# Optimization experiments

Hardware: AMD Instinct MI355X
Metric: run time of the kernel (lower is better)

## Reference

```python
import jax, jax.numpy as jnp
import numpy as np

B, N, C = 2, 2048, 1024
H = 16
HD = C // H
GH = C // 4  # spatial gate hidden dim


def setup_inputs() -> dict:
    key = jax.random.key(0)
    ks = jax.random.split(key, 10)
    s = 0.02
    return {
        "x": jax.random.normal(ks[0], (B, N, C), dtype=jnp.float32),
        "spatial_mask": jax.random.uniform(ks[1], (B, N), dtype=jnp.float32),
        # qkv Linear: weight [3C, C], bias [3C] (torch convention: y = x @ W.T + b)
        "qkv_w": jax.random.normal(ks[2], (3 * C, C), dtype=jnp.float32) * s,
        "qkv_b": jnp.zeros((3 * C,), dtype=jnp.float32),
        # output proj Linear: weight [C, C], bias [C]
        "proj_w": jax.random.normal(ks[3], (C, C), dtype=jnp.float32) * s,
        "proj_b": jnp.zeros((C,), dtype=jnp.float32),
        # spatial_gate: Linear(1, C//4) -> ReLU -> Linear(C//4, 1) -> Sigmoid
        "g1_w": jax.random.normal(ks[4], (GH, 1), dtype=jnp.float32) * 0.5,
        "g1_b": jnp.zeros((GH,), dtype=jnp.float32),
        "g2_w": jax.random.normal(ks[5], (1, GH), dtype=jnp.float32) * 0.1,
        "g2_b": jnp.zeros((1,), dtype=jnp.float32),
    }


def reference(x, spatial_mask, qkv_w, qkv_b, proj_w, proj_b, g1_w, g1_b, g2_w, g2_b):
    b, n, c = x.shape
    # QKV projection: [B, N, 3C] -> [3, B, H, N, HD]
    qkv = (x @ qkv_w.T + qkv_b).reshape(b, n, 3, H, HD).transpose(2, 0, 3, 1, 4)
    q, k, v = qkv[0], qkv[1], qkv[2]

    # scaled attention scores [B, H, N, N]
    attn = jnp.einsum("bhqd,bhkd->bhqk", q, k) * (HD ** -0.5)

    # spatial gate on the mask: scalar MLP applied per key position
    m = spatial_mask[..., None]                      # [B, N, 1]
    h = jax.nn.relu(m @ g1_w.T + g1_b)               # [B, N, GH]
    gate = jax.nn.sigmoid(h @ g2_w.T + g2_b)         # [B, N, 1]
    gate = gate[:, None, None, :, 0]                 # [B, 1, 1, N] broadcasts over heads & queries

    attn = jax.nn.softmax(attn * gate, axis=-1)

    out = jnp.einsum("bhqk,bhkd->bhqd", attn, v)     # [B, H, N, HD]
    out = out.transpose(0, 2, 1, 3).reshape(b, n, c) # [B, N, C]
    return out @ proj_w.T + proj_b
```

## Files before the change

### kernel.cpp

```cpp
#include <hip/hip_runtime.h>

#define H 16
#define NSEQ 2048
#define HD 64
#define CDIM 1024

typedef __attribute__((ext_vector_type(8))) short s8v;
typedef __attribute__((ext_vector_type(4))) float f4v;
typedef __attribute__((ext_vector_type(16))) float f16v;

#define GLL(g, l) __builtin_amdgcn_global_load_lds( \
    (const __attribute__((address_space(1))) void*)(g), \
    (__attribute__((address_space(3))) void*)(l), 16, 0, 0)

__device__ __forceinline__ short f2bf(float f) {
  union { float f; unsigned u; } x; x.f = f;
  unsigned r = (x.u + 0x7fffu + ((x.u >> 16) & 1u)) >> 16;
  return (short)r;
}
__device__ __forceinline__ short f2bf_fast(float f) {
  return (short)((__float_as_uint(f) + 0x8000u) >> 16);
}
__device__ __forceinline__ unsigned pk(float a, float b) {
  unsigned ua = __float_as_uint(a) + 0x8000u;
  unsigned ub = __float_as_uint(b) + 0x8000u;
  return __builtin_amdgcn_perm(ub, ua, 0x07060302);
}

__global__ __launch_bounds__(256) void cvt_gate_kernel(
    const float* __restrict__ a, const float* __restrict__ b, const float* __restrict__ c,
    const float* __restrict__ mask,
    const float* __restrict__ g1w, const float* __restrict__ g1b,
    const float* __restrict__ g2w, const float* __restrict__ g2b,
    short* __restrict__ oa, short* __restrict__ ob, short* __restrict__ oc,
    float* __restrict__ gate) {
  int i = blockIdx.x * 256 + threadIdx.x;
  if (i >= 2097152) {
    int j = i - 2097152;
    float m = mask[j];
    float acc = 0.f;
    for (int k = 0; k < 256; k++) {
      float h = fmaxf(m * g1w[k] + g1b[k], 0.f);
      acc += g2w[k] * h;
    }
    gate[j] = 1.f / (1.f + __expf(-(acc + g2b[0])));
    return;
  }
  const float* src; short* dst; int j;
  if (i < 1048576)      { src = a; dst = oa; j = i; }
  else if (i < 1835008) { src = b; dst = ob; j = i - 1048576; }
  else                  { src = c; dst = oc; j = i - 1835008; }
  float4 f = ((const float4*)src)[j];
  short4 s;
  s.x = f2bf(f.x); s.y = f2bf(f.y); s.z = f2bf(f.z); s.w = f2bf(f.w);
  ((short4*)dst)[j] = s;
}

__global__ __launch_bounds__(256) void gemm_qkv(const short* __restrict__ X,
    const short* __restrict__ W, const float* __restrict__ bias, const float* __restrict__ gate,
    short* __restrict__ qws, short* __restrict__ kws, short* __restrict__ vtws) {
  __shared__ __align__(16) short At[4096];
  __shared__ __align__(16) short Bt[4096];
  const int K = CDIM;
  int tid = threadIdx.x;
  int lane = tid & 63, w = tid >> 6;
  int quad = lane >> 4, l15 = lane & 15;
  int wm = w >> 1, wn = w & 1;
  long rowBase = (long)blockIdx.y * 128;
  long colBase = (long)blockIdx.x * 128;
  const f4v fz = {0.f, 0.f, 0.f, 0.f};
  f4v acc[4][4];
#pragma unroll
  for (int i = 0; i < 4; i++)
#pragma unroll
    for (int j = 0; j < 4; j++) acc[i][j] = fz;

  int j0 = tid, j1 = 256 + tid;
  int sr0 = j0 >> 2, sp0 = j0 & 3, sc0 = sp0 ^ ((sr0 >> 1) & 3);
  int sr1 = j1 >> 2, sp1 = j1 & 3, sc1 = sp1 ^ ((sr1 >> 1) & 3);
  const short* Xa = X + (rowBase + sr0) * K + sc0 * 8;
  const short* Xb = X + (rowBase + sr1) * K + sc1 * 8;
  const short* Wa = W + (colBase + sr0) * K + sc0 * 8;
  const short* Wb = W + (colBase + sr1) * K + sc1 * 8;

  for (int k0 = 0; k0 < K; k0 += 32) {
    __syncthreads();
    GLL(Xa + k0, &At[j0 * 8]);
    GLL(Xb + k0, &At[j1 * 8]);
    GLL(Wa + k0, &Bt[j0 * 8]);
    GLL(Wb + k0, &Bt[j1 * 8]);
    __syncthreads();
    s8v a[4], b[4];
#pragma unroll
    for (int mi = 0; mi < 4; mi++) {
      int row = wm * 64 + mi * 16 + l15;
      a[mi] = *(const s8v*)&At[row * 32 + ((quad ^ ((row >> 1) & 3)) * 8)];
    }
#pragma unroll
    for (int ni = 0; ni < 4; ni++) {
      int row = wn * 64 + ni * 16 + l15;
      b[ni] = *(const s8v*)&Bt[row * 32 + ((quad ^ ((row >> 1) & 3)) * 8)];
    }
#pragma unroll
    for (int mi = 0; mi < 4; mi++)
#pragma unroll
      for (int ni = 0; ni < 4; ni++)
        acc[mi][ni] = __builtin_amdgcn_mfma_f32_16x16x32_bf16(a[mi], b[ni], acc[mi][ni], 0, 0, 0);
  }
#pragma unroll
  for (int mi = 0; mi < 4; mi++) {
    int row = (int)rowBase + wm * 64 + mi * 16 + quad * 4;
    int bb = row >> 11, nn = row & 2047;
    f4v g4 = *(const f4v*)&gate[row];
    float gl[4];
#pragma unroll
    for (int r = 0; r < 4; r++) gl[r] = g4[r] * 1.44269504f;
#pragma unroll
    for (int ni = 0; ni < 4; ni++) {
      int col = (int)colBase + wn * 64 + ni * 16 + l15;
      int which = col >> 10, cc = col & 1023;
      int hh = cc >> 6, dd = cc & 63;
      float bcol = bias[col];
      if (which == 2) {
        short4 pv;
        pv.x = f2bf(acc[mi][ni][0] + bcol);
        pv.y = f2bf(acc[mi][ni][1] + bcol);
        pv.z = f2bf(acc[mi][ni][2] + bcol);
        pv.w = f2bf(acc[mi][ni][3] + bcol);
        *(short4*)&vtws[((bb * H + hh) * HD + dd) * NSEQ + nn] = pv;
      } else {
#pragma unroll
        for (int r = 0; r < 4; r++) {
          int idx = ((bb * H + hh) * NSEQ + nn + r) * HD + dd;
          float v = acc[mi][ni][r] + bcol;
          if (which == 0) qws[idx] = f2bf(v * 0.125f);
          else kws[idx] = f2bf(v * gl[r]);
        }
      }
    }
  }
}

__global__ __launch_bounds__(256) void gemm_proj(const short* __restrict__ X,
    const short* __restrict__ W, const float* __restrict__ bias, float* __restrict__ out) {
  __shared__ __align__(16) short At[2048];
  __shared__ __align__(16) short Bt[4096];
  const int K = CDIM;
  int tid = threadIdx.x;
  int lane = tid & 63, w = tid >> 6;
  int quad = lane >> 4, l15 = lane & 15;
  int wm = w >> 1, wn = w & 1;
  long rowBase = (long)blockIdx.y * 64;
  long colBase = (long)blockIdx.x * 128;
  const f4v fz = {0.f, 0.f, 0.f, 0.f};
  f4v acc[2][4];
#pragma unroll
  for (int i = 0; i < 2; i++)
#pragma unroll
    for (int j = 0; j < 4; j++) acc[i][j] = fz;

  int j0 = tid, j1 = 256 + tid;
  int sra = j0 >> 2, spa = j0 & 3, sca = spa ^ ((sra >> 1) & 3);
  int sr0 = j0 >> 2, sp0 = j0 & 3, sc0 = sp0 ^ ((sr0 >> 1) & 3);
  int sr1 = j1 >> 2, sp1 = j1 & 3, sc1 = sp1 ^ ((sr1 >> 1) & 3);
  const short* Xa = X + (rowBase + sra) * K + sca * 8;
  const short* Wa = W + (colBase + sr0) * K + sc0 * 8;
  const short* Wb = W + (colBase + sr1) * K + sc1 * 8;

  for (int k0 = 0; k0 < K; k0 += 32) {
    __syncthreads();
    GLL(Xa + k0, &At[j0 * 8]);
    GLL(Wa + k0, &Bt[j0 * 8]);
    GLL(Wb + k0, &Bt[j1 * 8]);
    __syncthreads();
    s8v a[2], b[4];
#pragma unroll
    for (int mi = 0; mi < 2; mi++) {
      int row = wm * 32 + mi * 16 + l15;
      a[mi] = *(const s8v*)&At[row * 32 + ((quad ^ ((row >> 1) & 3)) * 8)];
    }
#pragma unroll
    for (int ni = 0; ni < 4; ni++) {
      int row = wn * 64 + ni * 16 + l15;
      b[ni] = *(const s8v*)&Bt[row * 32 + ((quad ^ ((row >> 1) & 3)) * 8)];
    }
#pragma unroll
    for (int mi = 0; mi < 2; mi++)
#pragma unroll
      for (int ni = 0; ni < 4; ni++)
        acc[mi][ni] = __builtin_amdgcn_mfma_f32_16x16x32_bf16(a[mi], b[ni], acc[mi][ni], 0, 0, 0);
  }
#pragma unroll
  for (int mi = 0; mi < 2; mi++) {
    int row = (int)rowBase + wm * 32 + mi * 16 + quad * 4;
#pragma unroll
    for (int ni = 0; ni < 4; ni++) {
      int col = (int)colBase + wn * 64 + ni * 16 + l15;
      float bcol = bias[col];
#pragma unroll
      for (int r = 0; r < 4; r++)
        out[(long)(row + r) * CDIM + col] = acc[mi][ni][r] + bcol;
    }
  }
}

__global__ __launch_bounds__(256, 4) void attn_kernel(const short* __restrict__ qws,
    const short* __restrict__ kws, const short* __restrict__ vtws,
    short* __restrict__ attn_out) {
  __shared__ __align__(16) char smem[26624];
  short* Kt = (short*)smem;
  short* Vt = (short*)(smem + 8192);
  short* Pt = (short*)(smem + 16384);
  float* oscr = (float*)smem;
  float* lscr = (float*)(smem + 17408);
  float* linv = (float*)(smem + 17664);

  int tid = threadIdx.x;
  int lane = tid & 63, w = tid >> 6;
  int l31 = lane & 31, hf = lane >> 5;
  int wq = w >> 1, wk = w & 1;
  int sw = l31 & 7;
  int bh = blockIdx.x & 31, qt = blockIdx.x >> 5;
  int b = bh >> 4, head = bh & 15;
  int qbase = qt * 64;

  s8v qf[4];
  {
    const short* qp = qws + ((long)bh * NSEQ + qbase + wq * 32 + l31) * HD + hf * 8;
#pragma unroll
    for (int ds = 0; ds < 4; ds++) qf[ds] = *(const s8v*)&qp[ds * 16];
  }

  const f16v fz16 = {0.f,0.f,0.f,0.f,0.f,0.f,0.f,0.f,0.f,0.f,0.f,0.f,0.f,0.f,0.f,0.f};
  f16v oacc[2] = {fz16, fz16};
  float l_r = 0.f;

  int r8 = lane >> 3, c8 = lane & 7;
  int row0 = w * 16 + r8, row1 = row0 + 8;
  const short* kg0 = kws + ((long)bh * NSEQ + row0) * HD + (c8 ^ (row0 & 7)) * 8;
  const short* kg1 = kws + ((long)bh * NSEQ + row1) * HD + (c8 ^ (row1 & 7)) * 8;
  const short* vg0 = vtws + ((long)bh * HD + row0) * NSEQ + (c8 ^ (row0 & 7)) * 8;
  const short* vg1 = vtws + ((long)bh * HD + row1) * NSEQ + (c8 ^ (row1 & 7)) * 8;
  short* kl0 = Kt + (w * 16) * 64;
  short* kl1 = Kt + (w * 16 + 8) * 64;
  short* vl0 = Vt + (w * 16) * 64;
  short* vl1 = Vt + (w * 16 + 8) * 64;

  const short* myKrow = Kt + (wk * 32 + l31) * 64;
  short* myP = Pt + (w * 32 + l31) * 40;

  for (int kb = 0; kb < NSEQ; kb += 64) {
    __syncthreads();
    GLL(kg0 + (long)kb * HD, kl0);
    GLL(kg1 + (long)kb * HD, kl1);
    GLL(vg0 + kb, vl0);
    GLL(vg1 + kb, vl1);
    __syncthreads();

    f16v s = fz16;
#pragma unroll
    for (int ds = 0; ds < 4; ds++) {
      s8v ak = *(const s8v*)&myKrow[((2 * ds + hf) ^ sw) * 8];
      s = __builtin_amdgcn_mfma_f32_32x32x16_bf16(ak, qf[ds], s, 0, 0, 0);
    }
    float p[16];
#pragma unroll
    for (int i = 0; i < 16; i++) p[i] = __builtin_amdgcn_exp2f(s[i]);
    float ls = 0.f;
#pragma unroll
    for (int i = 0; i < 16; i++) ls += p[i];
    ls += __shfl_xor(ls, 32);
    l_r += ls;
#pragma unroll
    for (int q = 0; q < 4; q++) {
      uint2 wv;
      wv.x = pk(p[4 * q], p[4 * q + 1]);
      wv.y = pk(p[4 * q + 2], p[4 * q + 3]);
      *(uint2*)&myP[8 * q + 4 * hf] = wv;
    }
#pragma unroll
    for (int ks = 0; ks < 2; ks++) {
      s8v ap = *(const s8v*)&myP[ks * 16 + hf * 8];
#pragma unroll
      for (int nt = 0; nt < 2; nt++) {
        s8v bv = *(const s8v*)&Vt[(nt * 32 + l31) * 64 + (((4 * wk + 2 * ks + hf) ^ sw) * 8)];
        oacc[nt] = __builtin_amdgcn_mfma_f32_32x32x16_bf16(ap, bv, oacc[nt], 0, 0, 0);
      }
    }
  }

  __syncthreads();
  if (wk == 1) {
    lscr[wq * 32 + l31] = l_r;
#pragma unroll
    for (int nt = 0; nt < 2; nt++)
#pragma unroll
      for (int q = 0; q < 4; q++) {
        f4v t = {oacc[nt][4 * q], oacc[nt][4 * q + 1],
                 oacc[nt][4 * q + 2], oacc[nt][4 * q + 3]};
        *(f4v*)&oscr[(nt * 32 + l31) * 68 + wq * 32 + 8 * q + 4 * hf] = t;
      }
  }
  __syncthreads();
  if (wk == 0) {
    float lt = l_r + lscr[wq * 32 + l31];
    linv[wq * 32 + l31] = __builtin_amdgcn_rcpf(lt);
#pragma unroll
    for (int nt = 0; nt < 2; nt++) {
      int c = head * HD + nt * 32 + l31;
#pragma unroll
      for (int q = 0; q < 4; q++) {
        int rowbase = wq * 32 + 8 * q + 4 * hf;
        f4v part = *(const f4v*)&oscr[(nt * 32 + l31) * 68 + rowbase];
        f4v li = *(const f4v*)&linv[rowbase];
#pragma unroll
        for (int r = 0; r < 4; r++) {
          float val = (oacc[nt][4 * q + r] + part[r]) * li[r];
          int n = qbase + rowbase + r;
          attn_out[((long)b * NSEQ + n) * CDIM + c] = f2bf_fast(val);
        }
      }
    }
  }
}

extern "C" void kernel_launch(void* const* d_in, const int* in_sizes, int n_in,
                              void* d_out, int out_size, void* d_ws, size_t ws_size,
                              hipStream_t stream) {
  const float* x     = (const float*)d_in[0];
  const float* mask  = (const float*)d_in[1];
  const float* qkvw  = (const float*)d_in[2];
  const float* qkvb  = (const float*)d_in[3];
  const float* projw = (const float*)d_in[4];
  const float* projb = (const float*)d_in[5];
  const float* g1w   = (const float*)d_in[6];
  const float* g1b   = (const float*)d_in[7];
  const float* g2w   = (const float*)d_in[8];
  const float* g2b   = (const float*)d_in[9];
  float* out = (float*)d_out;

  char* ws = (char*)d_ws;
  short* x_bf    = (short*)(ws);
  short* w_qkv   = (short*)(ws + 8388608);
  short* w_proj  = (short*)(ws + 14680064);
  short* q_ws    = (short*)(ws + 16777216);
  short* k_ws    = (short*)(ws + 25165824);
  short* vt_ws   = (short*)(ws + 33554432);
  short* attn_bf = (short*)(ws + 41943040);
  float* gate    = (float*)(ws + 50331648);

  cvt_gate_kernel<<<8208, 256, 0, stream>>>(x, qkvw, projw, mask, g1w, g1b, g2w, g2b,
                                            x_bf, w_qkv, w_proj, gate);

  dim3 gq(24, 32);
  gemm_qkv<<<gq, 256, 0, stream>>>(x_bf, w_qkv, qkvb, gate, q_ws, k_ws, vt_ws);

  attn_kernel<<<1024, 256, 0, stream>>>(q_ws, k_ws, vt_ws, attn_bf);

  dim3 gp(8, 64);
  gemm_proj<<<gp, 256, 0, stream>>>(attn_bf, w_proj, projb, out);
}
```

Baseline: 219.3 us.

## Double-buffer GEMM and attention tiles, restructure attention to two-wave blocks

```diff
diff --git a/kernel.cpp b/kernel.cpp
--- a/kernel.cpp
+++ b/kernel.cpp
@@ -59,15 +59,15 @@
 __global__ __launch_bounds__(256) void gemm_qkv(const short* __restrict__ X,
     const short* __restrict__ W, const float* __restrict__ bias, const float* __restrict__ gate,
     short* __restrict__ qws, short* __restrict__ kws, short* __restrict__ vtws) {
-  __shared__ __align__(16) short At[4096];
-  __shared__ __align__(16) short Bt[4096];
+  __shared__ __align__(16) short Ft[8192];
+  __shared__ __align__(16) short Tt[8192];
   const int K = CDIM;
   int tid = threadIdx.x;
   int lane = tid & 63, w = tid >> 6;
   int quad = lane >> 4, l15 = lane & 15;
   int wm = w >> 1, wn = w & 1;
-  long rowBase = (long)blockIdx.y * 128;
-  long colBase = (long)blockIdx.x * 128;
+  long featBase = (long)blockIdx.x * 128;
+  long tokBase  = (long)blockIdx.y * 128;
   const f4v fz = {0.f, 0.f, 0.f, 0.f};
   f4v acc[4][4];
 #pragma unroll
@@ -78,28 +78,37 @@
   int j0 = tid, j1 = 256 + tid;
   int sr0 = j0 >> 2, sp0 = j0 & 3, sc0 = sp0 ^ ((sr0 >> 1) & 3);
   int sr1 = j1 >> 2, sp1 = j1 & 3, sc1 = sp1 ^ ((sr1 >> 1) & 3);
-  const short* Xa = X + (rowBase + sr0) * K + sc0 * 8;
-  const short* Xb = X + (rowBase + sr1) * K + sc1 * 8;
-  const short* Wa = W + (colBase + sr0) * K + sc0 * 8;
-  const short* Wb = W + (colBase + sr1) * K + sc1 * 8;
-
-  for (int k0 = 0; k0 < K; k0 += 32) {
-    __syncthreads();
-    GLL(Xa + k0, &At[j0 * 8]);
-    GLL(Xb + k0, &At[j1 * 8]);
-    GLL(Wa + k0, &Bt[j0 * 8]);
-    GLL(Wb + k0, &Bt[j1 * 8]);
+  const short* Wa = W + (featBase + sr0) * K + sc0 * 8;
+  const short* Wb = W + (featBase + sr1) * K + sc1 * 8;
+  const short* Xa = X + (tokBase + sr0) * K + sc0 * 8;
+  const short* Xb = X + (tokBase + sr1) * K + sc1 * 8;
+
+  GLL(Wa, &Ft[j0 * 8]);
+  GLL(Wb, &Ft[j1 * 8]);
+  GLL(Xa, &Tt[j0 * 8]);
+  GLL(Xb, &Tt[j1 * 8]);
+
+  for (int it = 0; it < 32; it++) {
+    int cur = (it & 1) * 4096;
     __syncthreads();
     s8v a[4], b[4];
 #pragma unroll
     for (int mi = 0; mi < 4; mi++) {
       int row = wm * 64 + mi * 16 + l15;
-      a[mi] = *(const s8v*)&At[row * 32 + ((quad ^ ((row >> 1) & 3)) * 8)];
+      a[mi] = *(const s8v*)&Ft[cur + row * 32 + ((quad ^ ((row >> 1) & 3)) * 8)];
     }
 #pragma unroll
     for (int ni = 0; ni < 4; ni++) {
       int row = wn * 64 + ni * 16 + l15;
-      b[ni] = *(const s8v*)&Bt[row * 32 + ((quad ^ ((row >> 1) & 3)) * 8)];
+      b[ni] = *(const s8v*)&Tt[cur + row * 32 + ((quad ^ ((row >> 1) & 3)) * 8)];
+    }
+    if (it < 31) {
+      int nb = 4096 - cur;
+      int k0 = (it + 1) * 32;
+      GLL(Wa + k0, &Ft[nb + j0 * 8]);
+      GLL(Wb + k0, &Ft[nb + j1 * 8]);
+      GLL(Xa + k0, &Tt[nb + j0 * 8]);
+      GLL(Xb + k0, &Tt[nb + j1 * 8]);
     }
 #pragma unroll
     for (int mi = 0; mi < 4; mi++)
@@ -109,33 +118,33 @@
   }
 #pragma unroll
   for (int mi = 0; mi < 4; mi++) {
-    int row = (int)rowBase + wm * 64 + mi * 16 + quad * 4;
-    int bb = row >> 11, nn = row & 2047;
-    f4v g4 = *(const f4v*)&gate[row];
-    float gl[4];
-#pragma unroll
-    for (int r = 0; r < 4; r++) gl[r] = g4[r] * 1.44269504f;
+    int feat0 = (int)featBase + wm * 64 + mi * 16 + quad * 4;
+    int which = feat0 >> 10, cc = feat0 & 1023;
+    int hh = cc >> 6, dd = cc & 63;
+    f4v b4 = *(const f4v*)&bias[feat0];
 #pragma unroll
     for (int ni = 0; ni < 4; ni++) {
-      int col = (int)colBase + wn * 64 + ni * 16 + l15;
-      int which = col >> 10, cc = col & 1023;
-      int hh = cc >> 6, dd = cc & 63;
-      float bcol = bias[col];
-      if (which == 2) {
+      int token = (int)tokBase + wn * 64 + ni * 16 + l15;
+      int bb = token >> 11, nn = token & 2047;
+      if (which == 0) {
         short4 pv;
-        pv.x = f2bf(acc[mi][ni][0] + bcol);
-        pv.y = f2bf(acc[mi][ni][1] + bcol);
-        pv.z = f2bf(acc[mi][ni][2] + bcol);
-        pv.w = f2bf(acc[mi][ni][3] + bcol);
-        *(short4*)&vtws[((bb * H + hh) * HD + dd) * NSEQ + nn] = pv;
+        pv.x = f2bf((acc[mi][ni][0] + b4[0]) * 0.125f);
+        pv.y = f2bf((acc[mi][ni][1] + b4[1]) * 0.125f);
+        pv.z = f2bf((acc[mi][ni][2] + b4[2]) * 0.125f);
+        pv.w = f2bf((acc[mi][ni][3] + b4[3]) * 0.125f);
+        *(short4*)&qws[((bb * H + hh) * NSEQ + nn) * HD + dd] = pv;
+      } else if (which == 1) {
+        float gl = gate[token] * 1.44269504f;
+        short4 pv;
+        pv.x = f2bf((acc[mi][ni][0] + b4[0]) * gl);
+        pv.y = f2bf((acc[mi][ni][1] + b4[1]) * gl);
+        pv.z = f2bf((acc[mi][ni][2] + b4[2]) * gl);
+        pv.w = f2bf((acc[mi][ni][3] + b4[3]) * gl);
+        *(short4*)&kws[((bb * H + hh) * NSEQ + nn) * HD + dd] = pv;
       } else {
 #pragma unroll
-        for (int r = 0; r < 4; r++) {
-          int idx = ((bb * H + hh) * NSEQ + nn + r) * HD + dd;
-          float v = acc[mi][ni][r] + bcol;
-          if (which == 0) qws[idx] = f2bf(v * 0.125f);
-          else kws[idx] = f2bf(v * gl[r]);
-        }
+        for (int r = 0; r < 4; r++)
+          vtws[((bb * H + hh) * HD + dd + r) * NSEQ + nn] = f2bf(acc[mi][ni][r] + b4[r]);
       }
     }
   }
@@ -143,8 +152,8 @@
 
 __global__ __launch_bounds__(256) void gemm_proj(const short* __restrict__ X,
     const short* __restrict__ W, const float* __restrict__ bias, float* __restrict__ out) {
-  __shared__ __align__(16) short At[2048];
-  __shared__ __align__(16) short Bt[4096];
+  __shared__ __align__(16) short At[4096];
+  __shared__ __align__(16) short Bt[8192];
   const int K = CDIM;
   int tid = threadIdx.x;
   int lane = tid & 63, w = tid >> 6;
@@ -160,29 +169,36 @@
     for (int j = 0; j < 4; j++) acc[i][j] = fz;
 
   int j0 = tid, j1 = 256 + tid;
-  int sra = j0 >> 2, spa = j0 & 3, sca = spa ^ ((sra >> 1) & 3);
   int sr0 = j0 >> 2, sp0 = j0 & 3, sc0 = sp0 ^ ((sr0 >> 1) & 3);
   int sr1 = j1 >> 2, sp1 = j1 & 3, sc1 = sp1 ^ ((sr1 >> 1) & 3);
-  const short* Xa = X + (rowBase + sra) * K + sca * 8;
+  const short* Xa = X + (rowBase + sr0) * K + sc0 * 8;
   const short* Wa = W + (colBase + sr0) * K + sc0 * 8;
   const short* Wb = W + (colBase + sr1) * K + sc1 * 8;
 
-  for (int k0 = 0; k0 < K; k0 += 32) {
-    __syncthreads();
-    GLL(Xa + k0, &At[j0 * 8]);
-    GLL(Wa + k0, &Bt[j0 * 8]);
-    GLL(Wb + k0, &Bt[j1 * 8]);
+  GLL(Xa, &At[j0 * 8]);
+  GLL(Wa, &Bt[j0 * 8]);
+  GLL(Wb, &Bt[j1 * 8]);
+
+  for (int it = 0; it < 32; it++) {
+    int curA = (it & 1) * 2048, curB = (it & 1) * 4096;
     __syncthreads();
     s8v a[2], b[4];
 #pragma unroll
     for (int mi = 0; mi < 2; mi++) {
       int row = wm * 32 + mi * 16 + l15;
-      a[mi] = *(const s8v*)&At[row * 32 + ((quad ^ ((row >> 1) & 3)) * 8)];
+      a[mi] = *(const s8v*)&At[curA + row * 32 + ((quad ^ ((row >> 1) & 3)) * 8)];
     }
 #pragma unroll
     for (int ni = 0; ni < 4; ni++) {
       int row = wn * 64 + ni * 16 + l15;
-      b[ni] = *(const s8v*)&Bt[row * 32 + ((quad ^ ((row >> 1) & 3)) * 8)];
+      b[ni] = *(const s8v*)&Bt[curB + row * 32 + ((quad ^ ((row >> 1) & 3)) * 8)];
+    }
+    if (it < 31) {
+      int nbA = 2048 - curA, nbB = 4096 - curB;
+      int k0 = (it + 1) * 32;
+      GLL(Xa + k0, &At[nbA + j0 * 8]);
+      GLL(Wa + k0, &Bt[nbB + j0 * 8]);
+      GLL(Wb + k0, &Bt[nbB + j1 * 8]);
     }
 #pragma unroll
     for (int mi = 0; mi < 2; mi++)
@@ -204,123 +220,154 @@
   }
 }
 
-__global__ __launch_bounds__(256, 4) void attn_kernel(const short* __restrict__ qws,
+__global__ __launch_bounds__(128, 2) void attn_kernel(const short* __restrict__ qws,
     const short* __restrict__ kws, const short* __restrict__ vtws,
     short* __restrict__ attn_out) {
-  __shared__ __align__(16) char smem[26624];
-  short* Kt = (short*)smem;
-  short* Vt = (short*)(smem + 8192);
-  short* Pt = (short*)(smem + 16384);
-  float* oscr = (float*)smem;
-  float* lscr = (float*)(smem + 17408);
-  float* linv = (float*)(smem + 17664);
+  __shared__ __align__(16) char smem[32768];
+  short* KB = (short*)smem;
+  short* VB = (short*)smem + 8192;
 
   int tid = threadIdx.x;
-  int lane = tid & 63, w = tid >> 6;
+  int lane = tid & 63;
+  int wk = tid >> 6;
   int l31 = lane & 31, hf = lane >> 5;
-  int wq = w >> 1, wk = w & 1;
-  int sw = l31 & 7;
   int bh = blockIdx.x & 31, qt = blockIdx.x >> 5;
   int b = bh >> 4, head = bh & 15;
   int qbase = qt * 64;
 
-  s8v qf[4];
+  s8v qf[2][4];
   {
-    const short* qp = qws + ((long)bh * NSEQ + qbase + wq * 32 + l31) * HD + hf * 8;
-#pragma unroll
-    for (int ds = 0; ds < 4; ds++) qf[ds] = *(const s8v*)&qp[ds * 16];
+    const short* qp = qws + ((long)bh * NSEQ + qbase + l31) * HD + hf * 8;
+#pragma unroll
+    for (int rt = 0; rt < 2; rt++)
+#pragma unroll
+      for (int ds = 0; ds < 4; ds++)
+        qf[rt][ds] = *(const s8v*)&qp[rt * 32 * HD + ds * 16];
   }
 
   const f16v fz16 = {0.f,0.f,0.f,0.f,0.f,0.f,0.f,0.f,0.f,0.f,0.f,0.f,0.f,0.f,0.f,0.f};
-  f16v oacc[2] = {fz16, fz16};
-  float l_r = 0.f;
+  f16v oacc[2][2];
+#pragma unroll
+  for (int rt = 0; rt < 2; rt++)
+#pragma unroll
+    for (int nt = 0; nt < 2; nt++) oacc[rt][nt] = fz16;
+  float l_r[2] = {0.f, 0.f};
 
   int r8 = lane >> 3, c8 = lane & 7;
-  int row0 = w * 16 + r8, row1 = row0 + 8;
-  const short* kg0 = kws + ((long)bh * NSEQ + row0) * HD + (c8 ^ (row0 & 7)) * 8;
-  const short* kg1 = kws + ((long)bh * NSEQ + row1) * HD + (c8 ^ (row1 & 7)) * 8;
-  const short* vg0 = vtws + ((long)bh * HD + row0) * NSEQ + (c8 ^ (row0 & 7)) * 8;
-  const short* vg1 = vtws + ((long)bh * HD + row1) * NSEQ + (c8 ^ (row1 & 7)) * 8;
-  short* kl0 = Kt + (w * 16) * 64;
-  short* kl1 = Kt + (w * 16 + 8) * 64;
-  short* vl0 = Vt + (w * 16) * 64;
-  short* vl1 = Vt + (w * 16 + 8) * 64;
-
-  const short* myKrow = Kt + (wk * 32 + l31) * 64;
-  short* myP = Pt + (w * 32 + l31) * 40;
-
-  for (int kb = 0; kb < NSEQ; kb += 64) {
+  const short* kg[4];
+  const short* vg[4];
+#pragma unroll
+  for (int g = 0; g < 4; g++) {
+    int row = wk * 32 + g * 8 + r8;
+    int sc = c8 ^ r8;
+    kg[g] = kws + ((long)bh * NSEQ + row) * HD + sc * 8;
+    vg[g] = vtws + ((long)bh * HD + row) * NSEQ + sc * 8;
+  }
+
+#pragma unroll
+  for (int g = 0; g < 4; g++) {
+    GLL(kg[g], KB + (wk * 32 + g * 8) * 64 + lane * 8);
+    GLL(vg[g], VB + (wk * 32 + g * 8) * 64 + lane * 8);
+  }
+
+  for (int it = 0; it < 32; it++) {
+    int cur = (it & 1) * 4096;
     __syncthreads();
-    GLL(kg0 + (long)kb * HD, kl0);
-    GLL(kg1 + (long)kb * HD, kl1);
-    GLL(vg0 + kb, vl0);
-    GLL(vg1 + kb, vl1);
-    __syncthreads();
-
-    f16v s = fz16;
-#pragma unroll
-    for (int ds = 0; ds < 4; ds++) {
-      s8v ak = *(const s8v*)&myKrow[((2 * ds + hf) ^ sw) * 8];
-      s = __builtin_amdgcn_mfma_f32_32x32x16_bf16(ak, qf[ds], s, 0, 0, 0);
-    }
-    float p[16];
-#pragma unroll
-    for (int i = 0; i < 16; i++) p[i] = __builtin_amdgcn_exp2f(s[i]);
-    float ls = 0.f;
-#pragma unroll
-    for (int i = 0; i < 16; i++) ls += p[i];
-    ls += __shfl_xor(ls, 32);
-    l_r += ls;
-#pragma unroll
-    for (int q = 0; q < 4; q++) {
-      uint2 wv;
-      wv.x = pk(p[4 * q], p[4 * q + 1]);
-      wv.y = pk(p[4 * q + 2], p[4 * q + 3]);
-      *(uint2*)&myP[8 * q + 4 * hf] = wv;
-    }
-#pragma unroll
-    for (int ks = 0; ks < 2; ks++) {
-      s8v ap = *(const s8v*)&myP[ks * 16 + hf * 8];
-#pragma unroll
-      for (int nt = 0; nt < 2; nt++) {
-        s8v bv = *(const s8v*)&Vt[(nt * 32 + l31) * 64 + (((4 * wk + 2 * ks + hf) ^ sw) * 8)];
-        oacc[nt] = __builtin_amdgcn_mfma_f32_32x32x16_bf16(ap, bv, oacc[nt], 0, 0, 0);
+    const short* Kc = KB + cur;
+    const short* Vc = VB + cur;
+    s8v ak[4];
+#pragma unroll
+    for (int ds = 0; ds < 4; ds++)
+      ak[ds] = *(const s8v*)&Kc[(wk * 32 + l31) * 64 + (((2 * ds + hf) ^ (l31 & 7)) * 8)];
+    s8v av[2][2];
+#pragma unroll
+    for (int nt = 0; nt < 2; nt++)
+#pragma unroll
+      for (int ks = 0; ks < 2; ks++)
+        av[nt][ks] = *(const s8v*)&Vc[(nt * 32 + l31) * 64 + (((wk * 4 + ks * 2 + hf) ^ (l31 & 7)) * 8)];
+    if (it < 31) {
+      int nb = 4096 - cur;
+      long koff = (long)(it + 1) * 64 * HD;
+      int voff = (it + 1) * 64;
+#pragma unroll
+      for (int g = 0; g < 4; g++) {
+        GLL(kg[g] + koff, KB + nb + (wk * 32 + g * 8) * 64 + lane * 8);
+        GLL(vg[g] + voff, VB + nb + (wk * 32 + g * 8) * 64 + lane * 8);
+      }
+    }
+#pragma unroll
+    for (int rt = 0; rt < 2; rt++) {
+      f16v s = fz16;
+#pragma unroll
+      for (int ds = 0; ds < 4; ds++)
+        s = __builtin_amdgcn_mfma_f32_32x32x16_bf16(ak[ds], qf[rt][ds], s, 0, 0, 0);
+      float p[16];
+#pragma unroll
+      for (int i = 0; i < 16; i++) p[i] = __builtin_amdgcn_exp2f(s[i]);
+      float ls = 0.f;
+#pragma unroll
+      for (int i = 0; i < 16; i++) ls += p[i];
+      ls += __shfl_xor(ls, 32);
+      l_r[rt] += ls;
+      unsigned Dp[4][2];
+#pragma unroll
+      for (int g = 0; g < 4; g++) {
+        Dp[g][0] = pk(p[4 * g], p[4 * g + 1]);
+        Dp[g][1] = pk(p[4 * g + 2], p[4 * g + 3]);
+      }
+#pragma unroll
+      for (int ks = 0; ks < 2; ks++) {
+        unsigned send0 = hf ? Dp[2 * ks][0] : Dp[2 * ks + 1][0];
+        unsigned send1 = hf ? Dp[2 * ks][1] : Dp[2 * ks + 1][1];
+        unsigned own0  = hf ? Dp[2 * ks + 1][0] : Dp[2 * ks][0];
+        unsigned own1  = hf ? Dp[2 * ks + 1][1] : Dp[2 * ks][1];
+        unsigned recv0 = (unsigned)__shfl_xor((int)send0, 32);
+        unsigned recv1 = (unsigned)__shfl_xor((int)send1, 32);
+        union { unsigned u[4]; s8v v; } bb;
+        bb.u[0] = hf ? recv0 : own0;
+        bb.u[1] = hf ? recv1 : own1;
+        bb.u[2] = hf ? own0 : recv0;
+        bb.u[3] = hf ? own1 : recv1;
+#pragma unroll
+        for (int nt = 0; nt < 2; nt++)
+          oacc[rt][nt] = __builtin_amdgcn_mfma_f32_32x32x16_bf16(av[nt][ks], bb.v, oacc[rt][nt], 0, 0, 0);
       }
     }
   }
 
   __syncthreads();
-  if (wk == 1) {
-    lscr[wq * 32 + l31] = l_r;
+  float* od = (float*)smem;
+  float* ld = (float*)(smem + 17408);
+  {
+    int rt = 1 - wk;
 #pragma unroll
     for (int nt = 0; nt < 2; nt++)
 #pragma unroll
-      for (int q = 0; q < 4; q++) {
-        f4v t = {oacc[nt][4 * q], oacc[nt][4 * q + 1],
-                 oacc[nt][4 * q + 2], oacc[nt][4 * q + 3]};
-        *(f4v*)&oscr[(nt * 32 + l31) * 68 + wq * 32 + 8 * q + 4 * hf] = t;
-      }
+      for (int g = 0; g < 4; g++) {
+        f4v t = {oacc[rt][nt][4 * g], oacc[rt][nt][4 * g + 1],
+                 oacc[rt][nt][4 * g + 2], oacc[rt][nt][4 * g + 3]};
+        *(f4v*)&od[rt * 2176 + l31 * 68 + nt * 32 + 8 * g + 4 * hf] = t;
+      }
+    ld[rt * 32 + l31] = l_r[rt];
   }
   __syncthreads();
-  if (wk == 0) {
-    float lt = l_r + lscr[wq * 32 + l31];
-    linv[wq * 32 + l31] = __builtin_amdgcn_rcpf(lt);
-#pragma unroll
-    for (int nt = 0; nt < 2; nt++) {
-      int c = head * HD + nt * 32 + l31;
-#pragma unroll
-      for (int q = 0; q < 4; q++) {
-        int rowbase = wq * 32 + 8 * q + 4 * hf;
-        f4v part = *(const f4v*)&oscr[(nt * 32 + l31) * 68 + rowbase];
-        f4v li = *(const f4v*)&linv[rowbase];
-#pragma unroll
-        for (int r = 0; r < 4; r++) {
-          float val = (oacc[nt][4 * q + r] + part[r]) * li[r];
-          int n = qbase + rowbase + r;
-          attn_out[((long)b * NSEQ + n) * CDIM + c] = f2bf_fast(val);
-        }
-      }
-    }
+  {
+    int rt = wk;
+    float lt = l_r[rt] + ld[rt * 32 + l31];
+    float li = __builtin_amdgcn_rcpf(lt);
+    long outbase = ((long)b * NSEQ + qbase + rt * 32 + l31) * CDIM + head * HD;
+#pragma unroll
+    for (int nt = 0; nt < 2; nt++)
+#pragma unroll
+      for (int g = 0; g < 4; g++) {
+        f4v part = *(const f4v*)&od[rt * 2176 + l31 * 68 + nt * 32 + 8 * g + 4 * hf];
+        short4 pv;
+        pv.x = f2bf_fast((oacc[rt][nt][4 * g]     + part[0]) * li);
+        pv.y = f2bf_fast((oacc[rt][nt][4 * g + 1] + part[1]) * li);
+        pv.z = f2bf_fast((oacc[rt][nt][4 * g + 2] + part[2]) * li);
+        pv.w = f2bf_fast((oacc[rt][nt][4 * g + 3] + part[3]) * li);
+        *(short4*)&attn_out[outbase + nt * 32 + 8 * g + 4 * hf] = pv;
+      }
   }
 }
 
@@ -355,7 +402,7 @@
   dim3 gq(24, 32);
   gemm_qkv<<<gq, 256, 0, stream>>>(x_bf, w_qkv, qkvb, gate, q_ws, k_ws, vt_ws);
 
-  attn_kernel<<<1024, 256, 0, stream>>>(q_ws, k_ws, vt_ws, attn_bf);
+  attn_kernel<<<1024, 128, 0, stream>>>(q_ws, k_ws, vt_ws, attn_bf);
 
   dim3 gp(8, 64);
   gemm_proj<<<gp, 256, 0, stream>>>(attn_bf, w_proj, projb, out);
```

Measured after the change: 305.4 us. +39.3%, slower.
